# Kernel tuning notes

Hardware: AMD Instinct MI355X
Metric: run time of the kernel (lower is better)

Reference implementation:

```python
import jax, jax.numpy as jnp
import numpy as np

SHIFT = 3
SHIFT2 = 1
POOL_K = 9
MAX_LEN = 16384
BATCH = 256


def _avg_pool1d(x, k, s):
    # x: [..., L] -> VALID average pool over last axis
    acc = jax.lax.reduce_window(x, 0.0, jax.lax.add,
                                (1,) * (x.ndim - 1) + (k,),
                                (1,) * (x.ndim - 1) + (s,), 'VALID')
    return acc / k


def _max_pool1d(x, k, s):
    return jax.lax.reduce_window(x, -jnp.inf, jax.lax.max,
                                 (1,) * (x.ndim - 1) + (k,),
                                 (1,) * (x.ndim - 1) + (s,), 'VALID')


def _upsample_nearest(x, size):
    # torch nn.Upsample(mode='nearest') to target length `size`
    m = x.shape[-1]
    idx = (jnp.arange(size) * m) // size
    return x[..., idx]


def setup_inputs() -> dict:
    key = jax.random.key(0)
    x = jax.random.normal(key, (BATCH, MAX_LEN), dtype=jnp.float32)
    return {"x": x}


def reference(x) -> jnp.ndarray:
    # First derivatives: fixed conv [[-1],[1]] over (rolled, original) row pairs
    # is exactly diff_d = x - roll(x, 2^d).  [B, shift, L]
    deriv1 = jnp.stack([x - jnp.roll(x, 1 << d, axis=-1) for d in range(SHIFT)], axis=1)
    # Second derivatives from the first diff channel (deriv1[:, 0]).
    d0 = deriv1[:, 0]
    deriv2 = jnp.stack([d0 - jnp.roll(d0, 1 << d, axis=-1) for d in range(SHIFT2)], axis=1)
    res = jnp.concatenate([deriv1, deriv2], axis=1)  # [B, shift+shift2, L]
    # Crop the wrapped-around prefix.
    off = max(1 << (SHIFT - 1), 1 << (SHIFT2 - 1))
    res = res[:, :, off:]
    # AvgPool1d(kernel=poolKernel, stride=1)
    res = _avg_pool1d(res, POOL_K, 1)  # [B, C, width]
    width = res.shape[-1]
    # MultiScale: four pool+upsample+residual branches, concat on channel dim.
    branches = [
        _upsample_nearest(_avg_pool1d(res, POOL_K, 1), width) + res,
        _upsample_nearest(_avg_pool1d(res, POOL_K, POOL_K), width) + res,
        _upsample_nearest(_max_pool1d(res, POOL_K, 1), width) + res,
        _upsample_nearest(_max_pool1d(res, POOL_K, POOL_K), width) + res,
    ]
    return jnp.concatenate(branches, axis=1)  # [B, 4*C, width]
```

## Files before the change

kernel.cpp:

```cpp
#include <hip/hip_runtime.h>

#define MAX_LEN 16384
#define RES_LEN 16372
#define NSEG    8
#define SEG     2048

__global__ __launch_bounds__(256, 7)
void derive_kernel(const float* __restrict__ x, float* __restrict__ out) {
    const int hw = blockIdx.x;
    const int lg = ((hw & 7) << 10) | (hw >> 3);
    const int b = lg >> 5;
    const int c = (lg >> 3) & 3;
    const int s = lg & 7;

    const float*  __restrict__ xr  = x + (size_t)b * MAX_LEN;
    const float4* __restrict__ xr4 = (const float4*)xr;

    const unsigned i0     = (unsigned)s * SEG;
    const unsigned i_last = (s == NSEG - 1) ? (RES_LEN - 1) : (i0 + SEG - 1);
    const int      nq     = (s == NSEG - 1) ? 509 : 512;
    const unsigned p1_i0  = (i0 * 16364u) / 16372u;
    const unsigned p2_i0  = (i0 * 1819u)  / 16372u;
    const unsigned p1_lst = (i_last * 16364u) / 16372u;
    const unsigned p2_lst = (i_last * 1819u)  / 16372u;
    const unsigned j_lo   = min(p1_i0, 9u * p2_i0);
    const unsigned j_lo_al = j_lo & ~3u;
    const unsigned j_hi   = max(p1_lst, 9u * p2_lst) + 8u;
    const int      nqw    = (int)((j_hi - j_lo_al + 1u + 3u) >> 2);
    const int      xqb    = (int)(j_lo_al >> 2);
    const int      np2    = (int)(p2_lst - p2_i0 + 1u);

    __shared__ float4 resS4[524];
    __shared__ float  a2S[232];
    __shared__ float  m2S[232];
    float* resS = (float*)resS4;

    const float inv9 = 1.0f / 9.0f;
    const int tid = threadIdx.x;

    for (int g = tid; g < nqw; g += 256) {
        const int gi = xqb + g;
        float4 A  = xr4[gi];
        float4 B4 = xr4[min(gi + 1, 4095)];
        float4 C4 = xr4[min(gi + 2, 4095)];
        float4 D4 = xr4[min(gi + 3, 4095)];
        float xv[16];
        xv[0]=A.x;  xv[1]=A.y;  xv[2]=A.z;  xv[3]=A.w;
        xv[4]=B4.x; xv[5]=B4.y; xv[6]=B4.z; xv[7]=B4.w;
        xv[8]=C4.x; xv[9]=C4.y; xv[10]=C4.z; xv[11]=C4.w;
        xv[12]=D4.x; xv[13]=D4.y; xv[14]=D4.z; xv[15]=D4.w;
        float rr[4];
        if (c == 0) {
            #pragma unroll
            for (int j = 0; j < 4; ++j) rr[j] = (xv[j+12] - xv[j+3]) * inv9;
        } else if (c == 1) {
            #pragma unroll
            for (int j = 0; j < 4; ++j) rr[j] = ((xv[j+12] + xv[j+11]) - (xv[j+3] + xv[j+2])) * inv9;
        } else if (c == 2) {
            #pragma unroll
            for (int j = 0; j < 4; ++j) rr[j] = ((xv[j+9] + xv[j+10] + xv[j+11] + xv[j+12])
                                               - (xv[j] + xv[j+1] + xv[j+2] + xv[j+3])) * inv9;
        } else {
            #pragma unroll
            for (int j = 0; j < 4; ++j) rr[j] = ((xv[j+12] - xv[j+11]) - (xv[j+3] - xv[j+2])) * inv9;
        }
        float4 rv; rv.x = rr[0]; rv.y = rr[1]; rv.z = rr[2]; rv.w = rr[3];
        resS4[g] = rv;
    }
    __syncthreads();

    for (int t = tid; t < np2; t += 256) {
        const int j0 = (int)(9u * (p2_i0 + (unsigned)t) - j_lo_al);
        float sm = resS[j0], mm = resS[j0];
        #pragma unroll
        for (int k = 1; k < 9; ++k) { float v = resS[j0 + k]; sm += v; mm = fmaxf(mm, v); }
        a2S[t] = sm * inv9; m2S[t] = mm;
    }
    __syncthreads();

    float* outBase = out + ((size_t)b * 16 + c) * RES_LEN;
    float4* o0p = (float4*)(outBase);
    float4* o1p = (float4*)(outBase + 4 * RES_LEN);
    float4* o2p = (float4*)(outBase + 8 * RES_LEN);
    float4* o3p = (float4*)(outBase + 12 * RES_LEN);
    const int gq0 = (int)(i0 >> 2);

    for (int t = tid; t < nq; t += 256) {
        const int gq = gq0 + t;
        const unsigned iq0 = 4u * (unsigned)gq;
        const unsigned p1_0 = (iq0 * 16364u) / 16372u;
        const unsigned p1_1 = ((iq0 + 1u) * 16364u) / 16372u;
        const unsigned p1_2 = ((iq0 + 2u) * 16364u) / 16372u;
        const unsigned p1_3 = ((iq0 + 3u) * 16364u) / 16372u;
        const unsigned p2_0 = (iq0 * 1819u) / 16372u;
        const unsigned p2_1 = ((iq0 + 1u) * 1819u) / 16372u;
        const unsigned p2_2 = ((iq0 + 2u) * 1819u) / 16372u;
        const unsigned p2_3 = ((iq0 + 3u) * 1819u) / 16372u;

        const unsigned li0 = p1_0 - j_lo_al;
        const unsigned q   = li0 >> 2;
        const unsigned o0  = li0 & 3u;
        const unsigned o1  = (p1_1 - j_lo_al) - 4u * q;
        const unsigned o2  = (p1_2 - j_lo_al) - 4u * q;
        const unsigned o3  = (p1_3 - j_lo_al) - 4u * q;

        float4 W0 = resS4[q], W1 = resS4[q + 1], W2 = resS4[q + 2], W3 = resS4[q + 3];
        float w[16];
        w[0]=W0.x;  w[1]=W0.y;  w[2]=W0.z;  w[3]=W0.w;
        w[4]=W1.x;  w[5]=W1.y;  w[6]=W1.z;  w[7]=W1.w;
        w[8]=W2.x;  w[9]=W2.y;  w[10]=W2.z; w[11]=W2.w;
        w[12]=W3.x; w[13]=W3.y; w[14]=W3.z; w[15]=W3.w;

        float s_[7];
        s_[0] = ((((((((w[0] + w[1]) + w[2]) + w[3]) + w[4]) + w[5]) + w[6]) + w[7]) + w[8]);
        #pragma unroll
        for (int e = 1; e < 7; ++e) s_[e] = s_[e - 1] - w[e - 1] + w[e + 8];

        float suf[7];
        suf[6] = fmaxf(fmaxf(w[6], w[7]), w[8]);
        #pragma unroll
        for (int u = 5; u >= 0; --u) suf[u] = fmaxf(w[u], suf[u + 1]);
        float pre[15];
        pre[8] = w[8];
        #pragma unroll
        for (int u = 9; u < 15; ++u) pre[u] = fmaxf(pre[u - 1], w[u]);
        float m_[7];
        #pragma unroll
        for (int o = 0; o < 7; ++o) m_[o] = fmaxf(suf[o], pre[o + 8]);

        float sum0 = s_[0], sum1 = s_[0], sum2 = s_[0], sum3 = s_[0];
        float mx0  = m_[0], mx1  = m_[0], mx2  = m_[0], mx3  = m_[0];
        #pragma unroll
        for (int e = 1; e <= 3; ++e) { bool t_ = (o0 >= (unsigned)e); sum0 = t_ ? s_[e] : sum0; mx0 = t_ ? m_[e] : mx0; }
        #pragma unroll
        for (int e = 1; e <= 4; ++e) { bool t_ = (o1 >= (unsigned)e); sum1 = t_ ? s_[e] : sum1; mx1 = t_ ? m_[e] : mx1; }
        #pragma unroll
        for (int e = 1; e <= 5; ++e) { bool t_ = (o2 >= (unsigned)e); sum2 = t_ ? s_[e] : sum2; mx2 = t_ ? m_[e] : mx2; }
        #pragma unroll
        for (int e = 1; e <= 6; ++e) { bool t_ = (o3 >= (unsigned)e); sum3 = t_ ? s_[e] : sum3; mx3 = t_ ? m_[e] : mx3; }

        const float4 R = resS4[(iq0 - j_lo_al) >> 2];

        const float a2l = a2S[p2_0 - p2_i0], a2h = a2S[p2_3 - p2_i0];
        const float m2l = m2S[p2_0 - p2_i0], m2h = m2S[p2_3 - p2_i0];
        const float a2_1 = (p2_1 != p2_0) ? a2h : a2l;
        const float a2_2 = (p2_2 != p2_0) ? a2h : a2l;
        const float m2_1 = (p2_1 != p2_0) ? m2h : m2l;
        const float m2_2 = (p2_2 != p2_0) ? m2h : m2l;

        float4 v0, v1, v2, v3;
        v0.x = sum0 * inv9 + R.x; v0.y = sum1 * inv9 + R.y; v0.z = sum2 * inv9 + R.z; v0.w = sum3 * inv9 + R.w;
        v1.x = a2l + R.x;         v1.y = a2_1 + R.y;        v1.z = a2_2 + R.z;        v1.w = a2h + R.w;
        v2.x = mx0 + R.x;         v2.y = mx1 + R.y;         v2.z = mx2 + R.z;         v2.w = mx3 + R.w;
        v3.x = m2l + R.x;         v3.y = m2_1 + R.y;        v3.z = m2_2 + R.z;        v3.w = m2h + R.w;

        o0p[gq] = v0; o1p[gq] = v1; o2p[gq] = v2; o3p[gq] = v3;
    }
}

extern "C" void kernel_launch(void* const* d_in, const int* in_sizes, int n_in,
                              void* d_out, int out_size, void* d_ws, size_t ws_size,
                              hipStream_t stream) {
    const float* x = (const float*)d_in[0];
    float* out = (float*)d_out;
    derive_kernel<<<dim3(256 * 4 * NSEG), dim3(256), 0, stream>>>(x, out);
}
```

Baseline: 66.51 us.

## Split output quads into constant-offset regimes with templated fast paths

The upsample index p1 = i*16364/16372 differs from i by a constant D inside long runs. The code computes the run boundaries analytically and processes each run with a template specialised on the sub-word offset. This removes the per-quad divisions for p1 and the select chains over seven candidate sums and maxes; boundary quads fall back to the general path. It also changes the block index mapping to a plain linear order and lowers the occupancy hint from 7 to 6, which may change cache locality and register allocation.

```diff
diff --git a/kernel.cpp b/kernel.cpp
--- a/kernel.cpp
+++ b/kernel.cpp
@@ -5,27 +5,89 @@
 #define NSEG    8
 #define SEG     2048
 
-__global__ __launch_bounds__(256, 7)
+template<int O0>
+__device__ void fast_regime(
+    int gA, int gB, int tid, unsigned D, unsigned j_lo_al, unsigned p2_i0,
+    const float4* __restrict__ resS4, const float* __restrict__ a2S,
+    const float* __restrict__ m2S,
+    float4* __restrict__ o0p, float4* __restrict__ o1p,
+    float4* __restrict__ o2p, float4* __restrict__ o3p)
+{
+    const float inv9 = 1.0f / 9.0f;
+    for (int g = gA + tid; g <= gB; g += 256) {
+        const unsigned iq0 = 4u * (unsigned)g;
+        const unsigned li0 = iq0 - D - j_lo_al;
+        const unsigned q   = li0 >> 2;
+        float4 W0 = resS4[q], W1 = resS4[q + 1], W2 = resS4[q + 2], W3 = resS4[q + 3];
+        float w[16];
+        w[0]=W0.x;  w[1]=W0.y;  w[2]=W0.z;  w[3]=W0.w;
+        w[4]=W1.x;  w[5]=W1.y;  w[6]=W1.z;  w[7]=W1.w;
+        w[8]=W2.x;  w[9]=W2.y;  w[10]=W2.z; w[11]=W2.w;
+        w[12]=W3.x; w[13]=W3.y; w[14]=W3.z; w[15]=W3.w;
+
+        float S0 = ((((((((w[O0]+w[O0+1])+w[O0+2])+w[O0+3])+w[O0+4])+w[O0+5])+w[O0+6])+w[O0+7])+w[O0+8]);
+        float S1 = S0 - w[O0]     + w[O0+9];
+        float S2 = S1 - w[O0+1]   + w[O0+10];
+        float S3 = S2 - w[O0+2]   + w[O0+11];
+
+        float c8 = w[O0+8];
+        float c7 = fmaxf(w[O0+7], c8);
+        float c6 = fmaxf(w[O0+6], c7);
+        float c5 = fmaxf(w[O0+5], c6);
+        float c4 = fmaxf(w[O0+4], c5);
+        float c3 = fmaxf(w[O0+3], c4);
+        float c2 = fmaxf(w[O0+2], c3);
+        float c1 = fmaxf(w[O0+1], c2);
+        float c0 = fmaxf(w[O0+0], c1);
+        float p10 = fmaxf(w[O0+9], w[O0+10]);
+        float mx0 = c0;
+        float mx1 = fmaxf(c1, w[O0+9]);
+        float mx2 = fmaxf(c2, p10);
+        float mx3 = fmaxf(c3, fmaxf(p10, w[O0+11]));
+
+        const float4 R = resS4[(iq0 - j_lo_al) >> 2];
+
+        const unsigned p2_0 = (iq0 * 1819u) / 16372u;
+        const unsigned p2_1 = ((iq0 + 1u) * 1819u) / 16372u;
+        const unsigned p2_2 = ((iq0 + 2u) * 1819u) / 16372u;
+        const unsigned p2_3 = ((iq0 + 3u) * 1819u) / 16372u;
+        const float a2l = a2S[p2_0 - p2_i0], a2h = a2S[p2_3 - p2_i0];
+        const float m2l = m2S[p2_0 - p2_i0], m2h = m2S[p2_3 - p2_i0];
+        const float a2_1 = (p2_1 != p2_0) ? a2h : a2l;
+        const float a2_2 = (p2_2 != p2_0) ? a2h : a2l;
+        const float m2_1 = (p2_1 != p2_0) ? m2h : m2l;
+        const float m2_2 = (p2_2 != p2_0) ? m2h : m2l;
+
+        float4 v0, v1, v2, v3;
+        v0.x = S0 * inv9 + R.x; v0.y = S1 * inv9 + R.y; v0.z = S2 * inv9 + R.z; v0.w = S3 * inv9 + R.w;
+        v1.x = a2l + R.x;       v1.y = a2_1 + R.y;      v1.z = a2_2 + R.z;      v1.w = a2h + R.w;
+        v2.x = mx0 + R.x;       v2.y = mx1 + R.y;       v2.z = mx2 + R.z;       v2.w = mx3 + R.w;
+        v3.x = m2l + R.x;       v3.y = m2_1 + R.y;      v3.z = m2_2 + R.z;      v3.w = m2h + R.w;
+
+        o0p[g] = v0; o1p[g] = v1; o2p[g] = v2; o3p[g] = v3;
+    }
+}
+
+__global__ __launch_bounds__(256, 6)
 void derive_kernel(const float* __restrict__ x, float* __restrict__ out) {
-    const int hw = blockIdx.x;
-    const int lg = ((hw & 7) << 10) | (hw >> 3);
-    const int b = lg >> 5;
-    const int c = (lg >> 3) & 3;
-    const int s = lg & 7;
+    const int bid = blockIdx.x;
+    const int b = bid >> 5;
+    const int c = (bid >> 3) & 3;
+    const int s = bid & 7;
 
     const float*  __restrict__ xr  = x + (size_t)b * MAX_LEN;
     const float4* __restrict__ xr4 = (const float4*)xr;
 
     const unsigned i0     = (unsigned)s * SEG;
     const unsigned i_last = (s == NSEG - 1) ? (RES_LEN - 1) : (i0 + SEG - 1);
-    const int      nq     = (s == NSEG - 1) ? 509 : 512;
     const unsigned p1_i0  = (i0 * 16364u) / 16372u;
     const unsigned p2_i0  = (i0 * 1819u)  / 16372u;
     const unsigned p1_lst = (i_last * 16364u) / 16372u;
     const unsigned p2_lst = (i_last * 1819u)  / 16372u;
-    const unsigned j_lo   = min(p1_i0, 9u * p2_i0);
+    const unsigned j_lo   = (p1_i0 < 9u * p2_i0) ? p1_i0 : 9u * p2_i0;
     const unsigned j_lo_al = j_lo & ~3u;
-    const unsigned j_hi   = max(p1_lst, 9u * p2_lst) + 8u;
+    const unsigned j_hi_a = p1_lst, j_hi_b = 9u * p2_lst;
+    const unsigned j_hi   = ((j_hi_a > j_hi_b) ? j_hi_a : j_hi_b) + 8u;
     const int      nqw    = (int)((j_hi - j_lo_al + 1u + 3u) >> 2);
     const int      xqb    = (int)(j_lo_al >> 2);
     const int      np2    = (int)(p2_lst - p2_i0 + 1u);
@@ -83,10 +145,13 @@
     float4* o1p = (float4*)(outBase + 4 * RES_LEN);
     float4* o2p = (float4*)(outBase + 8 * RES_LEN);
     float4* o3p = (float4*)(outBase + 12 * RES_LEN);
-    const int gq0 = (int)(i0 >> 2);
-
-    for (int t = tid; t < nq; t += 256) {
-        const int gq = gq0 + t;
+
+    const unsigned d_i0 = (8u * i0 + 16371u) / 16372u;
+    const unsigned bA = ((4093u * d_i0) >> 1) + 1u;
+    const unsigned bB = ((4093u * (d_i0 + 1u)) >> 1) + 1u;
+    const int nb = (bA <= i_last ? 1 : 0) + (bB <= i_last ? 1 : 0);
+
+    auto general_quad = [&](int gq) {
         const unsigned iq0 = 4u * (unsigned)gq;
         const unsigned p1_0 = (iq0 * 16364u) / 16372u;
         const unsigned p1_1 = ((iq0 + 1u) * 16364u) / 16372u;
@@ -96,26 +161,22 @@
         const unsigned p2_1 = ((iq0 + 1u) * 1819u) / 16372u;
         const unsigned p2_2 = ((iq0 + 2u) * 1819u) / 16372u;
         const unsigned p2_3 = ((iq0 + 3u) * 1819u) / 16372u;
-
         const unsigned li0 = p1_0 - j_lo_al;
         const unsigned q   = li0 >> 2;
         const unsigned o0  = li0 & 3u;
         const unsigned o1  = (p1_1 - j_lo_al) - 4u * q;
         const unsigned o2  = (p1_2 - j_lo_al) - 4u * q;
         const unsigned o3  = (p1_3 - j_lo_al) - 4u * q;
-
         float4 W0 = resS4[q], W1 = resS4[q + 1], W2 = resS4[q + 2], W3 = resS4[q + 3];
         float w[16];
         w[0]=W0.x;  w[1]=W0.y;  w[2]=W0.z;  w[3]=W0.w;
         w[4]=W1.x;  w[5]=W1.y;  w[6]=W1.z;  w[7]=W1.w;
         w[8]=W2.x;  w[9]=W2.y;  w[10]=W2.z; w[11]=W2.w;
         w[12]=W3.x; w[13]=W3.y; w[14]=W3.z; w[15]=W3.w;
-
         float s_[7];
         s_[0] = ((((((((w[0] + w[1]) + w[2]) + w[3]) + w[4]) + w[5]) + w[6]) + w[7]) + w[8]);
         #pragma unroll
         for (int e = 1; e < 7; ++e) s_[e] = s_[e - 1] - w[e - 1] + w[e + 8];
-
         float suf[7];
         suf[6] = fmaxf(fmaxf(w[6], w[7]), w[8]);
         #pragma unroll
@@ -127,7 +188,6 @@
         float m_[7];
         #pragma unroll
         for (int o = 0; o < 7; ++o) m_[o] = fmaxf(suf[o], pre[o + 8]);
-
         float sum0 = s_[0], sum1 = s_[0], sum2 = s_[0], sum3 = s_[0];
         float mx0  = m_[0], mx1  = m_[0], mx2  = m_[0], mx3  = m_[0];
         #pragma unroll
@@ -138,24 +198,43 @@
         for (int e = 1; e <= 5; ++e) { bool t_ = (o2 >= (unsigned)e); sum2 = t_ ? s_[e] : sum2; mx2 = t_ ? m_[e] : mx2; }
         #pragma unroll
         for (int e = 1; e <= 6; ++e) { bool t_ = (o3 >= (unsigned)e); sum3 = t_ ? s_[e] : sum3; mx3 = t_ ? m_[e] : mx3; }
-
         const float4 R = resS4[(iq0 - j_lo_al) >> 2];
-
         const float a2l = a2S[p2_0 - p2_i0], a2h = a2S[p2_3 - p2_i0];
         const float m2l = m2S[p2_0 - p2_i0], m2h = m2S[p2_3 - p2_i0];
         const float a2_1 = (p2_1 != p2_0) ? a2h : a2l;
         const float a2_2 = (p2_2 != p2_0) ? a2h : a2l;
         const float m2_1 = (p2_1 != p2_0) ? m2h : m2l;
         const float m2_2 = (p2_2 != p2_0) ? m2h : m2l;
-
         float4 v0, v1, v2, v3;
         v0.x = sum0 * inv9 + R.x; v0.y = sum1 * inv9 + R.y; v0.z = sum2 * inv9 + R.z; v0.w = sum3 * inv9 + R.w;
         v1.x = a2l + R.x;         v1.y = a2_1 + R.y;        v1.z = a2_2 + R.z;        v1.w = a2h + R.w;
         v2.x = mx0 + R.x;         v2.y = mx1 + R.y;         v2.z = mx2 + R.z;         v2.w = mx3 + R.w;
         v3.x = m2l + R.x;         v3.y = m2_1 + R.y;        v3.z = m2_2 + R.z;        v3.w = m2h + R.w;
-
         o0p[gq] = v0; o1p[gq] = v1; o2p[gq] = v2; o3p[gq] = v3;
-    }
+    };
+
+    auto dispatch = [&](unsigned D, int gA, int gB) {
+        switch ((4u - (D & 3u)) & 3u) {
+            case 0: fast_regime<0>(gA, gB, tid, D, j_lo_al, p2_i0, resS4, a2S, m2S, o0p, o1p, o2p, o3p); break;
+            case 1: fast_regime<1>(gA, gB, tid, D, j_lo_al, p2_i0, resS4, a2S, m2S, o0p, o1p, o2p, o3p); break;
+            case 2: fast_regime<2>(gA, gB, tid, D, j_lo_al, p2_i0, resS4, a2S, m2S, o0p, o1p, o2p, o3p); break;
+            default: fast_regime<3>(gA, gB, tid, D, j_lo_al, p2_i0, resS4, a2S, m2S, o0p, o1p, o2p, o3p); break;
+        }
+    };
+
+    {
+        const unsigned re = (nb >= 1) ? (bA - 1u) : i_last;
+        dispatch(d_i0, (int)((i0 + 3u) >> 2), ((int)re - 3) >> 2);
+    }
+    if (nb >= 1) {
+        const unsigned re = (nb >= 2) ? (bB - 1u) : i_last;
+        dispatch(d_i0 + 1u, (int)((bA + 3u) >> 2), ((int)re - 3) >> 2);
+    }
+    if (nb >= 2) {
+        dispatch(d_i0 + 2u, (int)((bB + 3u) >> 2), ((int)i_last - 3) >> 2);
+    }
+    if (nb >= 1 && (bA & 3u) && tid == 0) general_quad((int)(bA >> 2));
+    if (nb >= 2 && (bB & 3u) && tid == 1) general_quad((int)(bB >> 2));
 }
 
 extern "C" void kernel_launch(void* const* d_in, const int* in_sizes, int n_in,
```

Result: slower. 69.76 us (+4.9%).
